# Optimization experiments

Hardware: AMD Instinct MI355X
Metric: run time of the kernel (lower is better)

The kernel has to match this reference:

```python
import jax, jax.numpy as jnp
import numpy as np

NUM_SUBSPACES = 8
CODEBOOK_SIZE = 256
SUBSPACE_DIM = 96


def setup_inputs() -> dict:
    key = jax.random.key(0)
    k1, k2 = jax.random.split(key)
    embeddings = jax.random.normal(k1, (16, 4096, NUM_SUBSPACES * SUBSPACE_DIM), dtype=jnp.float32)
    codebooks = jax.random.normal(k2, (NUM_SUBSPACES, CODEBOOK_SIZE, SUBSPACE_DIM), dtype=jnp.float32)
    return {"embeddings": embeddings, "codebooks": codebooks}


def reference(embeddings, codebooks):
    # embeddings: [B, S, E] with E = M*d; codebooks: [M, K, d]
    B, S, E = embeddings.shape
    M, K, d = codebooks.shape
    # [N, M, d] -> [M, N, d] so each subspace is contiguous
    x = embeddings.reshape(B * S, M, d).transpose(1, 0, 2)
    x2 = jnp.sum(x * x, axis=-1, keepdims=True)              # [M, N, 1]
    c2 = jnp.sum(codebooks * codebooks, axis=-1)[:, None, :]  # [M, 1, K]
    xc = jnp.einsum('mnd,mkd->mnk', x, codebooks)             # [M, N, K]
    dist2 = x2 - 2.0 * xc + c2                                # [M, N, K]
    # argmin over codes (same result as cdist p=2 argmin since sqrt is monotone)
    idx = jnp.argmin(dist2, axis=-1)                          # [M, N]
    # gather nearest codewords per subspace
    quantized = codebooks[jnp.arange(M)[:, None], idx]        # [M, N, d]
    # reassemble: [N, M, d] -> [B, S, E]
    return quantized.transpose(1, 0, 2).reshape(B, S, E)
```

## Files before the change

kernel.cpp:

```cpp
#include <hip/hip_runtime.h>

typedef short   bf16x8 __attribute__((ext_vector_type(8)));
typedef unsigned short u16x8 __attribute__((ext_vector_type(8)));
typedef float   f32x16 __attribute__((ext_vector_type(16)));

constexpr int NSUB  = 8;
constexpr int NCODE = 256;
constexpr int SDIM  = 96;
constexpr int EMB   = NSUB * SDIM;
constexpr float C_SHIFT = 192.0f;
constexpr float THR = 0.02f;

constexpr int    CB_UNITS      = 8 * 6 * 2 * 64;
constexpr size_t WS_FRAG_BYTES = (size_t)NSUB * CB_UNITS * 16;
constexpr size_t WS_NEEDED     = WS_FRAG_BYTES + (size_t)NSUB * NCODE * 4;

__device__ __forceinline__ unsigned short f2bf(float v) {
    unsigned u = __builtin_bit_cast(unsigned, v);
    u = u + 0x7FFFu + ((u >> 16) & 1u);
    return (unsigned short)(u >> 16);
}
__device__ __forceinline__ float bf2f(unsigned short h) {
    unsigned u = ((unsigned)h) << 16;
    return __builtin_bit_cast(float, u);
}

__global__ __launch_bounds__(256) void pq_prep(const float* __restrict__ cb,
                                               unsigned short* __restrict__ wsf,
                                               float* __restrict__ wsc2)
{
    const int m   = (int)blockIdx.x;
    const int tid = (int)threadIdx.x;
    {
        const float* c = cb + ((size_t)m * NCODE + tid) * SDIM;
        double s = 0.0;
        for (int k = 0; k < SDIM; ++k) { double v = (double)c[k]; s += v * v; }
        wsc2[m * NCODE + tid] = (float)(0.5 * s + (double)C_SHIFT);
    }
    for (int i = 0; i < 24; ++i) {
        int u  = i * 256 + tid;
        int l  = u & 63;
        int c6 = u >> 6;
        int h  = c6 & 1; c6 >>= 1;
        int s  = c6 % 6;
        int t  = c6 / 6;
        int code = t * 32 + (l & 31);
        int k0   = s * 16 + (l >> 5) * 8;
        const float* src = cb + (size_t)m * NCODE * SDIM + (size_t)code * SDIM + k0;
        u16x8 o;
        #pragma unroll
        for (int j = 0; j < 8; ++j) {
            float v = -src[j];
            unsigned short hb = f2bf(v);
            o[j] = (h == 0) ? hb : f2bf(v - bf2f(hb));
        }
        *(u16x8*)(wsf + ((size_t)m * CB_UNITS + u) * 8) = o;
    }
}

__global__ __launch_bounds__(256, 3) void pq_mfma8(
    const float* __restrict__ emb,
    const float* __restrict__ cb,
    const unsigned short* __restrict__ wsf,
    const float* __restrict__ wsc2,
    float* __restrict__ out,
    int nrows,
    int rowblks)
{
    const int tid  = (int)threadIdx.x;
    const int lane = tid & 63;
    const int hib  = lane >> 5;
    const int widx = (int)blockIdx.x * 4 + (tid >> 6);
    if (widx >= NSUB * rowblks) return;
    const int m    = widx / rowblks;
    const int rb   = widx % rowblks;
    const int row0 = rb * 32;

    const unsigned short* wb = wsf + (size_t)m * CB_UNITS * 8;
    const float* c2p = wsc2 + m * NCODE;

    bf16x8 xh[6], xl[6];
    {
        int r = row0 + (lane & 31);
        if (r >= nrows) r = nrows - 1;
        const float* xr = emb + (size_t)r * EMB + m * SDIM + hib * 8;
        #pragma unroll
        for (int s = 0; s < 6; ++s) {
            float4 v0 = *(const float4*)(xr + s * 16);
            float4 v1 = *(const float4*)(xr + s * 16 + 4);
            float v[8] = { v0.x, v0.y, v0.z, v0.w, v1.x, v1.y, v1.z, v1.w };
            #pragma unroll
            for (int j = 0; j < 8; ++j) {
                unsigned short hb = f2bf(v[j]);
                xh[s][j] = (short)hb;
                xl[s][j] = (short)f2bf(v[j] - bf2f(hb));
            }
        }
    }

    float b1 = 3.4e38f, b2 = 3.4e38f;
    int   i1 = 1 << 30, i2 = 1 << 30;
    #pragma unroll 1
    for (int p = 0; p < 4; ++p) {
        const int t0 = p * 2, t1 = t0 + 1;
        f32x16 a0, a1;
        #pragma unroll
        for (int rq = 0; rq < 4; ++rq) {
            float4 q0 = *(const float4*)(c2p + t0 * 32 + rq * 8 + hib * 4);
            float4 q1 = *(const float4*)(c2p + t1 * 32 + rq * 8 + hib * 4);
            a0[rq*4+0]=q0.x; a0[rq*4+1]=q0.y; a0[rq*4+2]=q0.z; a0[rq*4+3]=q0.w;
            a1[rq*4+0]=q1.x; a1[rq*4+1]=q1.y; a1[rq*4+2]=q1.z; a1[rq*4+3]=q1.w;
        }
        #pragma unroll
        for (int s = 0; s < 6; ++s) {
            bf16x8 ah0 = *(const bf16x8*)(wb + (size_t)((((t0 * 6 + s) * 2) + 0) * 64 + lane) * 8);
            bf16x8 al0 = *(const bf16x8*)(wb + (size_t)((((t0 * 6 + s) * 2) + 1) * 64 + lane) * 8);
            bf16x8 ah1 = *(const bf16x8*)(wb + (size_t)((((t1 * 6 + s) * 2) + 0) * 64 + lane) * 8);
            bf16x8 al1 = *(const bf16x8*)(wb + (size_t)((((t1 * 6 + s) * 2) + 1) * 64 + lane) * 8);
            a0 = __builtin_amdgcn_mfma_f32_32x32x16_bf16(ah0, xh[s], a0, 0, 0, 0);
            a1 = __builtin_amdgcn_mfma_f32_32x32x16_bf16(ah1, xh[s], a1, 0, 0, 0);
            a0 = __builtin_amdgcn_mfma_f32_32x32x16_bf16(al0, xh[s], a0, 0, 0, 0);
            a1 = __builtin_amdgcn_mfma_f32_32x32x16_bf16(al1, xh[s], a1, 0, 0, 0);
            a0 = __builtin_amdgcn_mfma_f32_32x32x16_bf16(ah0, xl[s], a0, 0, 0, 0);
            a1 = __builtin_amdgcn_mfma_f32_32x32x16_bf16(ah1, xl[s], a1, 0, 0, 0);
        }
        #pragma unroll
        for (int r = 0; r < 16; ++r) {
            float sv = a0[r];
            int   kv = t0 * 32 + (r & 3) + 8 * (r >> 2) + hib * 4;
            if (sv < b1)      { b2 = b1; i2 = i1; b1 = sv; i1 = kv; }
            else if (sv < b2) { b2 = sv; i2 = kv; }
        }
        #pragma unroll
        for (int r = 0; r < 16; ++r) {
            float sv = a1[r];
            int   kv = t1 * 32 + (r & 3) + 8 * (r >> 2) + hib * 4;
            if (sv < b1)      { b2 = b1; i2 = i1; b1 = sv; i1 = kv; }
            else if (sv < b2) { b2 = sv; i2 = kv; }
        }
    }
    {
        float ob1 = __shfl_xor(b1, 32);
        int   oi1 = __shfl_xor(i1, 32);
        float ob2 = __shfl_xor(b2, 32);
        int   oi2 = __shfl_xor(i2, 32);
        bool o1_better = (ob1 < b1) || (ob1 == b1 && oi1 < i1);
        if (o1_better) {
            bool mine_better = (b1 < ob2) || (b1 == ob2 && i1 < oi2);
            if (mine_better) { b2 = b1; i2 = i1; } else { b2 = ob2; i2 = oi2; }
            b1 = ob1; i1 = oi1;
        } else {
            if ((ob1 < b2) || (ob1 == b2 && oi1 < i2)) { b2 = ob1; i2 = oi1; }
        }
    }

    {
        int grow = row0 + (lane & 31);
        if (lane < 32 && grow < nrows && (b2 - b1 < THR)) {
            const float* xr = emb + (size_t)grow * EMB + m * SDIM;
            const float* ca = cb + ((size_t)m * NCODE + i1) * SDIM;
            const float* cbv = cb + ((size_t)m * NCODE + i2) * SDIM;
            double da = 0.0, db = 0.0;
            for (int kk = 0; kk < SDIM; ++kk) {
                double ea = (double)xr[kk] - (double)ca[kk];
                double eb = (double)xr[kk] - (double)cbv[kk];
                da += ea * ea; db += eb * eb;
            }
            if (db < da || (db == da && i2 < i1)) i1 = i2;
        }
    }

    #pragma unroll
    for (int ii = 0; ii < 12; ++ii) {
        int Q = ii * 64 + lane;
        int r = Q / 24, f = Q % 24;
        int grow = row0 + r;
        int k = __shfl(i1, r);
        if (grow < nrows) {
            float4 v = *(const float4*)(cb + ((size_t)m * NCODE + k) * SDIM + f * 4);
            *(float4*)(out + (size_t)grow * EMB + m * SDIM + f * 4) = v;
        }
    }
}

__global__ __launch_bounds__(256) void pq_argmin_kernel(
    const float* __restrict__ emb, const float* __restrict__ cb,
    float* __restrict__ out, int nrows)
{
    const int m   = (int)(blockIdx.x & 7);
    const int row = (int)(blockIdx.x >> 3) * 256 + (int)threadIdx.x;
    const float* __restrict__ cbm = cb + (size_t)m * (NCODE * SDIM);
    __shared__ float half_c2[NCODE];
    {
        const int k = (int)threadIdx.x;
        const float* c = cbm + k * SDIM;
        float s = 0.f;
        #pragma unroll
        for (int i = 0; i < SDIM; i += 4) {
            const float4 v = *reinterpret_cast<const float4*>(c + i);
            s = fmaf(v.x, v.x, s); s = fmaf(v.y, v.y, s);
            s = fmaf(v.z, v.z, s); s = fmaf(v.w, v.w, s);
        }
        half_c2[k] = 0.5f * s;
    }
    __syncthreads();
    if (row >= nrows) return;
    float x[SDIM];
    {
        const float* xr = emb + (size_t)row * EMB + m * SDIM;
        #pragma unroll
        for (int i = 0; i < SDIM; i += 4) {
            const float4 v = *reinterpret_cast<const float4*>(xr + i);
            x[i+0] = v.x; x[i+1] = v.y; x[i+2] = v.z; x[i+3] = v.w;
        }
    }
    float best = 3.4e38f, best2 = 3.4e38f;
    int bestk = 0, bestk2 = 0;
    #pragma unroll 1
    for (int k = 0; k < NCODE; k += 4) {
        const float* c0 = cbm + (k + 0) * SDIM;
        const float* c1 = cbm + (k + 1) * SDIM;
        const float* c2 = cbm + (k + 2) * SDIM;
        const float* c3 = cbm + (k + 3) * SDIM;
        float a0 = 0.f, a1 = 0.f, a2 = 0.f, a3 = 0.f;
        #pragma unroll
        for (int i = 0; i < SDIM; i += 4) {
            const float4 v0 = *reinterpret_cast<const float4*>(c0 + i);
            const float4 v1 = *reinterpret_cast<const float4*>(c1 + i);
            const float4 v2 = *reinterpret_cast<const float4*>(c2 + i);
            const float4 v3 = *reinterpret_cast<const float4*>(c3 + i);
            a0 = fmaf(x[i+0], v0.x, a0); a0 = fmaf(x[i+1], v0.y, a0);
            a0 = fmaf(x[i+2], v0.z, a0); a0 = fmaf(x[i+3], v0.w, a0);
            a1 = fmaf(x[i+0], v1.x, a1); a1 = fmaf(x[i+1], v1.y, a1);
            a1 = fmaf(x[i+2], v1.z, a1); a1 = fmaf(x[i+3], v1.w, a1);
            a2 = fmaf(x[i+0], v2.x, a2); a2 = fmaf(x[i+1], v2.y, a2);
            a2 = fmaf(x[i+2], v2.z, a2); a2 = fmaf(x[i+3], v2.w, a2);
            a3 = fmaf(x[i+0], v3.x, a3); a3 = fmaf(x[i+1], v3.y, a3);
            a3 = fmaf(x[i+2], v3.z, a3); a3 = fmaf(x[i+3], v3.w, a3);
        }
        const float s[4] = { half_c2[k+0] - a0, half_c2[k+1] - a1,
                             half_c2[k+2] - a2, half_c2[k+3] - a3 };
        #pragma unroll
        for (int j = 0; j < 4; ++j) {
            if (s[j] < best)       { best2 = best; bestk2 = bestk; best = s[j]; bestk = k + j; }
            else if (s[j] < best2) { best2 = s[j]; bestk2 = k + j; }
        }
    }
    if (best2 - best < 0.02f) {
        const float* ca = cbm + bestk  * SDIM;
        const float* cbv = cbm + bestk2 * SDIM;
        double da = 0.0, db = 0.0;
        for (int i = 0; i < SDIM; ++i) {
            const double ea = (double)x[i] - (double)ca[i];
            const double eb = (double)x[i] - (double)cbv[i];
            da += ea * ea; db += eb * eb;
        }
        if (db < da || (db == da && bestk2 < bestk)) bestk = bestk2;
    }
    const float* cbest = cbm + bestk * SDIM;
    float* o = out + (size_t)row * EMB + m * SDIM;
    #pragma unroll
    for (int i = 0; i < SDIM; i += 4)
        *reinterpret_cast<float4*>(o + i) = *reinterpret_cast<const float4*>(cbest + i);
}

extern "C" void kernel_launch(void* const* d_in, const int* in_sizes, int n_in,
                              void* d_out, int out_size, void* d_ws, size_t ws_size,
                              hipStream_t stream) {
    const float* emb = (const float*)d_in[0];
    const float* cb  = (const float*)d_in[1];
    float* out = (float*)d_out;
    const int nrows = in_sizes[0] / EMB;

    if (ws_size < WS_NEEDED) {
        const int rowBlocks = (nrows + 255) / 256;
        pq_argmin_kernel<<<dim3(rowBlocks * NSUB), dim3(256), 0, stream>>>(emb, cb, out, nrows);
        return;
    }

    unsigned short* wsf = (unsigned short*)d_ws;
    float* wsc2 = (float*)((char*)d_ws + WS_FRAG_BYTES);

    pq_prep<<<dim3(NSUB), dim3(256), 0, stream>>>(cb, wsf, wsc2);

    const int rowblks = (nrows + 31) / 32;
    const int nwaves  = rowblks * NSUB;
    const int nb      = (nwaves + 3) / 4;
    pq_mfma8<<<dim3(nb), dim3(256), 0, stream>>>(emb, cb, wsf, wsc2, out, nrows, rowblks);
}
```

Before: 206.2 us.

## Process two 32-row tiles per wave to reuse codebook fragments

Each wave now handles 64 rows as two 32-row tiles (A and B). Every codebook fragment loaded from global memory feeds MFMAs for both tiles, which halves codebook fragment traffic per row and interleaves independent accumulator chains. The cost is roughly double the register use (four accumulators plus two sets of x fragments), and the occupancy hint in launch bounds is dropped, so occupancy may fall. The fp64 refinement and the output gather are widened to cover all 64 lanes and rows.

```diff
diff --git a/kernel.cpp b/kernel.cpp
--- a/kernel.cpp
+++ b/kernel.cpp
@@ -58,7 +58,7 @@
     }
 }
 
-__global__ __launch_bounds__(256, 3) void pq_mfma8(
+__global__ __launch_bounds__(256) void pq_mfma10(
     const float* __restrict__ emb,
     const float* __restrict__ cb,
     const unsigned short* __restrict__ wsf,
@@ -74,108 +74,154 @@
     if (widx >= NSUB * rowblks) return;
     const int m    = widx / rowblks;
     const int rb   = widx % rowblks;
-    const int row0 = rb * 32;
+    const int row0 = rb * 64;
 
     const unsigned short* wb = wsf + (size_t)m * CB_UNITS * 8;
     const float* c2p = wsc2 + m * NCODE;
 
-    bf16x8 xh[6], xl[6];
-    {
-        int r = row0 + (lane & 31);
-        if (r >= nrows) r = nrows - 1;
-        const float* xr = emb + (size_t)r * EMB + m * SDIM + hib * 8;
+    bf16x8 xhA[6], xlA[6], xhB[6], xlB[6];
+    {
+        int rA = row0 + (lane & 31);      if (rA >= nrows) rA = nrows - 1;
+        int rB = row0 + 32 + (lane & 31); if (rB >= nrows) rB = nrows - 1;
+        const float* xrA = emb + (size_t)rA * EMB + m * SDIM + hib * 8;
+        const float* xrB = emb + (size_t)rB * EMB + m * SDIM + hib * 8;
         #pragma unroll
         for (int s = 0; s < 6; ++s) {
-            float4 v0 = *(const float4*)(xr + s * 16);
-            float4 v1 = *(const float4*)(xr + s * 16 + 4);
-            float v[8] = { v0.x, v0.y, v0.z, v0.w, v1.x, v1.y, v1.z, v1.w };
+            float4 a0 = *(const float4*)(xrA + s * 16);
+            float4 a1 = *(const float4*)(xrA + s * 16 + 4);
+            float4 b0 = *(const float4*)(xrB + s * 16);
+            float4 b1 = *(const float4*)(xrB + s * 16 + 4);
+            float va[8] = { a0.x, a0.y, a0.z, a0.w, a1.x, a1.y, a1.z, a1.w };
+            float vb[8] = { b0.x, b0.y, b0.z, b0.w, b1.x, b1.y, b1.z, b1.w };
             #pragma unroll
             for (int j = 0; j < 8; ++j) {
-                unsigned short hb = f2bf(v[j]);
-                xh[s][j] = (short)hb;
-                xl[s][j] = (short)f2bf(v[j] - bf2f(hb));
+                unsigned short ha = f2bf(va[j]);
+                xhA[s][j] = (short)ha;
+                xlA[s][j] = (short)f2bf(va[j] - bf2f(ha));
+                unsigned short hbv = f2bf(vb[j]);
+                xhB[s][j] = (short)hbv;
+                xlB[s][j] = (short)f2bf(vb[j] - bf2f(hbv));
             }
         }
     }
 
-    float b1 = 3.4e38f, b2 = 3.4e38f;
-    int   i1 = 1 << 30, i2 = 1 << 30;
+    float b1A = 3.4e38f, b2A = 3.4e38f, b1B = 3.4e38f, b2B = 3.4e38f;
+    int   i1A = 1 << 30, i2A = 1 << 30, i1B = 1 << 30, i2B = 1 << 30;
     #pragma unroll 1
     for (int p = 0; p < 4; ++p) {
         const int t0 = p * 2, t1 = t0 + 1;
-        f32x16 a0, a1;
+        f32x16 a0A, a1A, a0B, a1B;
         #pragma unroll
         for (int rq = 0; rq < 4; ++rq) {
             float4 q0 = *(const float4*)(c2p + t0 * 32 + rq * 8 + hib * 4);
             float4 q1 = *(const float4*)(c2p + t1 * 32 + rq * 8 + hib * 4);
-            a0[rq*4+0]=q0.x; a0[rq*4+1]=q0.y; a0[rq*4+2]=q0.z; a0[rq*4+3]=q0.w;
-            a1[rq*4+0]=q1.x; a1[rq*4+1]=q1.y; a1[rq*4+2]=q1.z; a1[rq*4+3]=q1.w;
-        }
+            a0A[rq*4+0]=q0.x; a0A[rq*4+1]=q0.y; a0A[rq*4+2]=q0.z; a0A[rq*4+3]=q0.w;
+            a1A[rq*4+0]=q1.x; a1A[rq*4+1]=q1.y; a1A[rq*4+2]=q1.z; a1A[rq*4+3]=q1.w;
+        }
+        a0B = a0A; a1B = a1A;
         #pragma unroll
         for (int s = 0; s < 6; ++s) {
             bf16x8 ah0 = *(const bf16x8*)(wb + (size_t)((((t0 * 6 + s) * 2) + 0) * 64 + lane) * 8);
             bf16x8 al0 = *(const bf16x8*)(wb + (size_t)((((t0 * 6 + s) * 2) + 1) * 64 + lane) * 8);
             bf16x8 ah1 = *(const bf16x8*)(wb + (size_t)((((t1 * 6 + s) * 2) + 0) * 64 + lane) * 8);
             bf16x8 al1 = *(const bf16x8*)(wb + (size_t)((((t1 * 6 + s) * 2) + 1) * 64 + lane) * 8);
-            a0 = __builtin_amdgcn_mfma_f32_32x32x16_bf16(ah0, xh[s], a0, 0, 0, 0);
-            a1 = __builtin_amdgcn_mfma_f32_32x32x16_bf16(ah1, xh[s], a1, 0, 0, 0);
-            a0 = __builtin_amdgcn_mfma_f32_32x32x16_bf16(al0, xh[s], a0, 0, 0, 0);
-            a1 = __builtin_amdgcn_mfma_f32_32x32x16_bf16(al1, xh[s], a1, 0, 0, 0);
-            a0 = __builtin_amdgcn_mfma_f32_32x32x16_bf16(ah0, xl[s], a0, 0, 0, 0);
-            a1 = __builtin_amdgcn_mfma_f32_32x32x16_bf16(ah1, xl[s], a1, 0, 0, 0);
+            a0A = __builtin_amdgcn_mfma_f32_32x32x16_bf16(ah0, xhA[s], a0A, 0, 0, 0);
+            a0B = __builtin_amdgcn_mfma_f32_32x32x16_bf16(ah0, xhB[s], a0B, 0, 0, 0);
+            a1A = __builtin_amdgcn_mfma_f32_32x32x16_bf16(ah1, xhA[s], a1A, 0, 0, 0);
+            a1B = __builtin_amdgcn_mfma_f32_32x32x16_bf16(ah1, xhB[s], a1B, 0, 0, 0);
+            a0A = __builtin_amdgcn_mfma_f32_32x32x16_bf16(al0, xhA[s], a0A, 0, 0, 0);
+            a0B = __builtin_amdgcn_mfma_f32_32x32x16_bf16(al0, xhB[s], a0B, 0, 0, 0);
+            a1A = __builtin_amdgcn_mfma_f32_32x32x16_bf16(al1, xhA[s], a1A, 0, 0, 0);
+            a1B = __builtin_amdgcn_mfma_f32_32x32x16_bf16(al1, xhB[s], a1B, 0, 0, 0);
+            a0A = __builtin_amdgcn_mfma_f32_32x32x16_bf16(ah0, xlA[s], a0A, 0, 0, 0);
+            a0B = __builtin_amdgcn_mfma_f32_32x32x16_bf16(ah0, xlB[s], a0B, 0, 0, 0);
+            a1A = __builtin_amdgcn_mfma_f32_32x32x16_bf16(ah1, xlA[s], a1A, 0, 0, 0);
+            a1B = __builtin_amdgcn_mfma_f32_32x32x16_bf16(ah1, xlB[s], a1B, 0, 0, 0);
         }
         #pragma unroll
         for (int r = 0; r < 16; ++r) {
-            float sv = a0[r];
+            float sv = a0A[r];
             int   kv = t0 * 32 + (r & 3) + 8 * (r >> 2) + hib * 4;
-            if (sv < b1)      { b2 = b1; i2 = i1; b1 = sv; i1 = kv; }
-            else if (sv < b2) { b2 = sv; i2 = kv; }
+            if (sv < b1A)      { b2A = b1A; i2A = i1A; b1A = sv; i1A = kv; }
+            else if (sv < b2A) { b2A = sv; i2A = kv; }
         }
         #pragma unroll
         for (int r = 0; r < 16; ++r) {
-            float sv = a1[r];
+            float sv = a1A[r];
             int   kv = t1 * 32 + (r & 3) + 8 * (r >> 2) + hib * 4;
-            if (sv < b1)      { b2 = b1; i2 = i1; b1 = sv; i1 = kv; }
-            else if (sv < b2) { b2 = sv; i2 = kv; }
-        }
-    }
-    {
-        float ob1 = __shfl_xor(b1, 32);
-        int   oi1 = __shfl_xor(i1, 32);
-        float ob2 = __shfl_xor(b2, 32);
-        int   oi2 = __shfl_xor(i2, 32);
-        bool o1_better = (ob1 < b1) || (ob1 == b1 && oi1 < i1);
+            if (sv < b1A)      { b2A = b1A; i2A = i1A; b1A = sv; i1A = kv; }
+            else if (sv < b2A) { b2A = sv; i2A = kv; }
+        }
+        #pragma unroll
+        for (int r = 0; r < 16; ++r) {
+            float sv = a0B[r];
+            int   kv = t0 * 32 + (r & 3) + 8 * (r >> 2) + hib * 4;
+            if (sv < b1B)      { b2B = b1B; i2B = i1B; b1B = sv; i1B = kv; }
+            else if (sv < b2B) { b2B = sv; i2B = kv; }
+        }
+        #pragma unroll
+        for (int r = 0; r < 16; ++r) {
+            float sv = a1B[r];
+            int   kv = t1 * 32 + (r & 3) + 8 * (r >> 2) + hib * 4;
+            if (sv < b1B)      { b2B = b1B; i2B = i1B; b1B = sv; i1B = kv; }
+            else if (sv < b2B) { b2B = sv; i2B = kv; }
+        }
+    }
+    {
+        float ob1 = __shfl_xor(b1A, 32);
+        int   oi1 = __shfl_xor(i1A, 32);
+        float ob2 = __shfl_xor(b2A, 32);
+        int   oi2 = __shfl_xor(i2A, 32);
+        bool o1_better = (ob1 < b1A) || (ob1 == b1A && oi1 < i1A);
         if (o1_better) {
-            bool mine_better = (b1 < ob2) || (b1 == ob2 && i1 < oi2);
-            if (mine_better) { b2 = b1; i2 = i1; } else { b2 = ob2; i2 = oi2; }
-            b1 = ob1; i1 = oi1;
+            bool mine_better = (b1A < ob2) || (b1A == ob2 && i1A < oi2);
+            if (mine_better) { b2A = b1A; i2A = i1A; } else { b2A = ob2; i2A = oi2; }
+            b1A = ob1; i1A = oi1;
         } else {
-            if ((ob1 < b2) || (ob1 == b2 && oi1 < i2)) { b2 = ob1; i2 = oi1; }
-        }
-    }
-
-    {
-        int grow = row0 + (lane & 31);
-        if (lane < 32 && grow < nrows && (b2 - b1 < THR)) {
+            if ((ob1 < b2A) || (ob1 == b2A && oi1 < i2A)) { b2A = ob1; i2A = oi1; }
+        }
+    }
+    {
+        float ob1 = __shfl_xor(b1B, 32);
+        int   oi1 = __shfl_xor(i1B, 32);
+        float ob2 = __shfl_xor(b2B, 32);
+        int   oi2 = __shfl_xor(i2B, 32);
+        bool o1_better = (ob1 < b1B) || (ob1 == b1B && oi1 < i1B);
+        if (o1_better) {
+            bool mine_better = (b1B < ob2) || (b1B == ob2 && i1B < oi2);
+            if (mine_better) { b2B = b1B; i2B = i1B; } else { b2B = ob2; i2B = oi2; }
+            b1B = ob1; i1B = oi1;
+        } else {
+            if ((ob1 < b2B) || (ob1 == b2B && oi1 < i2B)) { b2B = ob1; i2B = oi1; }
+        }
+    }
+
+    float gb1 = (lane < 32) ? b1A : b1B;
+    float gb2 = (lane < 32) ? b2A : b2B;
+    int   gi1 = (lane < 32) ? i1A : i1B;
+    int   gi2 = (lane < 32) ? i2A : i2B;
+    {
+        int grow = row0 + lane;
+        if (grow < nrows && (gb2 - gb1 < THR)) {
             const float* xr = emb + (size_t)grow * EMB + m * SDIM;
-            const float* ca = cb + ((size_t)m * NCODE + i1) * SDIM;
-            const float* cbv = cb + ((size_t)m * NCODE + i2) * SDIM;
+            const float* ca = cb + ((size_t)m * NCODE + gi1) * SDIM;
+            const float* cbv = cb + ((size_t)m * NCODE + gi2) * SDIM;
             double da = 0.0, db = 0.0;
             for (int kk = 0; kk < SDIM; ++kk) {
                 double ea = (double)xr[kk] - (double)ca[kk];
                 double eb = (double)xr[kk] - (double)cbv[kk];
                 da += ea * ea; db += eb * eb;
             }
-            if (db < da || (db == da && i2 < i1)) i1 = i2;
+            if (db < da || (db == da && gi2 < gi1)) gi1 = gi2;
         }
     }
 
     #pragma unroll
-    for (int ii = 0; ii < 12; ++ii) {
+    for (int ii = 0; ii < 24; ++ii) {
         int Q = ii * 64 + lane;
         int r = Q / 24, f = Q % 24;
         int grow = row0 + r;
-        int k = __shfl(i1, r);
+        int k = __shfl(gi1, r);
         if (grow < nrows) {
             float4 v = *(const float4*)(cb + ((size_t)m * NCODE + k) * SDIM + f * 4);
             *(float4*)(out + (size_t)grow * EMB + m * SDIM + f * 4) = v;
@@ -283,8 +329,8 @@
 
     pq_prep<<<dim3(NSUB), dim3(256), 0, stream>>>(cb, wsf, wsc2);
 
-    const int rowblks = (nrows + 31) / 32;
+    const int rowblks = (nrows + 63) / 64;
     const int nwaves  = rowblks * NSUB;
     const int nb      = (nwaves + 3) / 4;
-    pq_mfma8<<<dim3(nb), dim3(256), 0, stream>>>(emb, cb, wsf, wsc2, out, nrows, rowblks);
-}
+    pq_mfma10<<<dim3(nb), dim3(256), 0, stream>>>(emb, cb, wsf, wsc2, out, nrows, rowblks);
+}
```

Measured after the change: 305.2 us. +48.0%, slower.
